# Performance work log

Hardware: AMD Instinct MI355X
Metric: run time of the kernel (lower is better)

The kernel has to match this reference:

```python
import jax, jax.numpy as jnp
import numpy as np

N, C, HEADS = 32768, 512, 8
CK = CV = C // 2   # key/value channels (= hidden//2 per AE.block1)
F2 = C // 2        # CAM in_features
BN_EPS = 1e-5


def _bn(x, p):
    # eval-mode BatchNorm2d on [n, c, w] (h=1 squeezed); p = [gamma, beta, mean, var] each [c]
    g, b, m, v = p
    inv = g / jnp.sqrt(v + BN_EPS)
    return (x - m[None, :, None]) * inv[None, :, None] + b[None, :, None]


def _conv(x, w):
    # 1x1 Conv2d (no bias) on [n, c, w]; w: [out_c, in_c]
    return jnp.einsum('ncw,oc->now', x, w)


def _block(x, y, ea_wk, ea_bk, ea_wq, ea_bq, ea_wv, ea_bv, ea_wr, ea_br,
           pool_w1, pool_bn1, pool_w2, pool_bn2,
           adapt_w1, adapt_bn1, adapt_w2, adapt_bn2,
           delta_w1, delta_bn1, delta_w2):
    # torch: input_ = stack([x, y]).permute([0,2,1]).unsqueeze(2) -> [2, C, 1, N]; we drop h=1 -> [2, C, N]
    inp = jnp.stack([x, y]).transpose(0, 2, 1)  # [2, C, N]

    # ---------------- EfficientAttention ----------------
    keys = _conv(inp, ea_wk) + ea_bk[None, :, None]      # [2, CK, N]
    queries = _conv(inp, ea_wq) + ea_bq[None, :, None]   # [2, CK, N]
    values = _conv(inp, ea_wv) + ea_bv[None, :, None]    # [2, CV, N]
    hk, hv = CK // HEADS, CV // HEADS
    K = jax.nn.softmax(keys.reshape(2, HEADS, hk, N), axis=-1)     # softmax over positions
    Q = jax.nn.softmax(queries.reshape(2, HEADS, hk, N), axis=2)   # softmax over head channels
    V = values.reshape(2, HEADS, hv, N)
    ctx = jnp.einsum('nhkw,nhvw->nhkv', K, V)                      # [2, H, hk, hv]
    att = jnp.einsum('nhkv,nhkw->nhvw', ctx, Q).reshape(2, CV, N)  # [2, CV, N]
    ea_full = _conv(att, ea_wr) + ea_br[None, :, None] + inp       # reprojection + residual
    ea_out = ((ea_full[0] + ea_full[1]) * 0.5).T                   # [N, C]

    # ---------------- CAM ----------------
    high = inp.mean(axis=2, keepdims=True)                 # AdaptiveAvgPool2d(1) -> [2, C, 1]
    high = _bn(_conv(high, pool_w1), pool_bn1)
    high = _bn(_conv(high, pool_w2), pool_bn2)             # [2, F2, 1]
    low = _bn(_conv(inp, adapt_w1), adapt_bn1)
    low = _bn(_conv(low, adapt_w2), adapt_bn2)             # [2, F2, N]
    # bilinear upsample of a 1x1 map == broadcast
    high_up = jnp.broadcast_to(high, (2, F2, N))
    concat = jnp.concatenate([low, high_up], axis=1)       # [2, 2*F2, N]
    d = _bn(_conv(concat, delta_w1), delta_bn1)
    delta = _conv(d, delta_w2)                             # [2, 2, N]: (dx, dy)
    # grid_sample of 1x1 `high`, zeros padding, align_corners=False; norm = [w/s, h/s] = [1, 1]
    gx = jnp.linspace(-1.0, 1.0, N)[None, :] + delta[:, 0]  # h_list + delta_x, [2, N]
    gy = -1.0 + delta[:, 1]                                 # linspace(-1,1,1) = -1
    ix, iy = gx * 0.5, gy * 0.5                             # unnormalized coords for W=H=1
    wgt = jnp.clip(1.0 - jnp.abs(ix), 0.0, 1.0) * jnp.clip(1.0 - jnp.abs(iy), 0.0, 1.0)  # [2, N]
    sampled = high * wgt[:, None, :]                        # [2, F2, N]
    cam_full = jnp.concatenate([sampled, low], axis=1)      # [2, 2*F2, N] == [2, C, N]
    cam_out = ((cam_full[0] + cam_full[1]) * 0.5).T         # [N, C]

    return (ea_out + cam_out) * 0.5                         # [N, C]


def setup_inputs() -> dict:
    key = jax.random.key(0)
    ks = iter(jax.random.split(key, 40))
    def rn(shape, s=0.05):
        return jax.random.normal(next(ks), shape, jnp.float32) * s
    def bn(c):
        p = jax.random.normal(next(ks), (4, c), jnp.float32) * 0.05
        p = p.at[0].add(1.0)                 # gamma ~ 1
        p = p.at[3].set(jnp.abs(p[3]) + 1.0)  # var > 0
        return p
    return {
        'x': jax.random.normal(next(ks), (N, C), jnp.float32),
        'y': jax.random.normal(next(ks), (N, C), jnp.float32),
        'ea_wk': rn((CK, C)), 'ea_bk': rn((CK,)),
        'ea_wq': rn((CK, C)), 'ea_bq': rn((CK,)),
        'ea_wv': rn((CV, C)), 'ea_bv': rn((CV,)),
        'ea_wr': rn((C, CV)), 'ea_br': rn((C,)),
        'pool_w1': rn((C, C)), 'pool_bn1': bn(C),
        'pool_w2': rn((F2, C)), 'pool_bn2': bn(F2),
        'adapt_w1': rn((C, C)), 'adapt_bn1': bn(C),
        'adapt_w2': rn((F2, C)), 'adapt_bn2': bn(F2),
        'delta_w1': rn((F2, 2 * F2)), 'delta_bn1': bn(F2),
        'delta_w2': rn((2, F2)),
    }


def reference(x, y, ea_wk, ea_bk, ea_wq, ea_bq, ea_wv, ea_bv, ea_wr, ea_br,
              pool_w1, pool_bn1, pool_w2, pool_bn2,
              adapt_w1, adapt_bn1, adapt_w2, adapt_bn2,
              delta_w1, delta_bn1, delta_w2):
    return _block(x, y, ea_wk, ea_bk, ea_wq, ea_bq, ea_wv, ea_bv, ea_wr, ea_br,
                  pool_w1, pool_bn1, pool_w2, pool_bn2,
                  adapt_w1, adapt_bn1, adapt_w2, adapt_bn2,
                  delta_w1, delta_bn1, delta_w2)
```

## Files before the change

### kernel.cpp

```cpp
#include <hip/hip_runtime.h>
#include <math.h>

#define B_CTXC   0
#define B_ZP     524288
#define B_COLS   526336
#define B_HIGH2  530432
#define B_CONSTD 532480
#define B_BIASO  532544
#define B_CPP    534592
#define B_CTXT   535616
#define B_WDD    568384
#define B_WDX    570432
#define B_WL     574528
#define B_WBIG   1098816
#define B_WKV    1639488
#define B_WR     2163776
#define B_PW1T   2425920
#define B_PW2T   3474496
#define B_D1BT   3998784

typedef __attribute__((ext_vector_type(8))) short bf16x8;
typedef __attribute__((ext_vector_type(4))) float f32x4;

#define MFMA(a, b, c) __builtin_amdgcn_mfma_f32_16x16x32_bf16(a, b, c, 0, 0, 0)
#define EVSWZ(row) ((((row) >> 1) & 3) << 4)

__device__ inline unsigned f2bfu(float f) {
  unsigned u = __float_as_uint(f);
  return (u + 0x7FFFu + ((u >> 16) & 1u)) >> 16;
}
__device__ inline unsigned pack2(float a, float b) { return f2bfu(a) | (f2bfu(b) << 16); }

__device__ inline void softmax_pack(f32x4 a0, f32x4 a1, const float* __restrict__ bq,
                                    int hh, int g, unsigned o[4]) {
  float q[8], e[8];
  float mx = -1e30f;
#pragma unroll
  for (int r = 0; r < 4; ++r) {
    q[r] = a0[r] + bq[hh * 32 + g * 4 + r];
    q[4 + r] = a1[r] + bq[hh * 32 + 16 + g * 4 + r];
    mx = fmaxf(mx, fmaxf(q[r], q[4 + r]));
  }
  mx = fmaxf(mx, __shfl_xor(mx, 16, 64));
  mx = fmaxf(mx, __shfl_xor(mx, 32, 64));
  float sm = 0.f;
#pragma unroll
  for (int r = 0; r < 8; ++r) { e[r] = __expf(q[r] - mx); sm += e[r]; }
  sm += __shfl_xor(sm, 16, 64);
  sm += __shfl_xor(sm, 32, 64);
  float inv = 1.f / sm;
  o[0] = pack2(e[0] * inv, e[1] * inv); o[1] = pack2(e[2] * inv, e[3] * inv);
  o[2] = pack2(e[4] * inv, e[5] * inv); o[3] = pack2(e[6] * inv, e[7] * inv);
}

__global__ __launch_bounds__(512) void kW1(
    const float* __restrict__ a1, const float* __restrict__ abn1,
    const float* __restrict__ a2, const float* __restrict__ abn2,
    char* __restrict__ wsb) {
  __shared__ float S1[512], F1[512], redu[512];
  const int t = threadIdx.x, o = blockIdx.x;
  float* wsf = (float*)wsb;
  {
    float gg = abn1[t], be = abn1[512 + t], mn = abn1[1024 + t], va = abn1[1536 + t];
    float s = gg * rsqrtf(va + 1e-5f);
    S1[t] = s; F1[t] = be - mn * s;
  }
  float g2 = abn2[o], be2 = abn2[256 + o], mn2 = abn2[512 + o], va2 = abn2[768 + o];
  float s2 = g2 * rsqrtf(va2 + 1e-5f);
  float f2v = be2 - mn2 * s2;
  __syncthreads();
  float acc = 0.f;
  const float* a2r = a2 + o * 512;
  for (int m = 0; m < 512; ++m) acc = fmaf(a2r[m] * S1[m], a1[m * 512 + t], acc);
  wsf[(B_WL / 4) + o * 512 + t] = s2 * acc;
  redu[t] = a2r[t] * F1[t];
  __syncthreads();
  for (int sft = 256; sft >= 1; sft >>= 1) {
    if (t < sft) redu[t] += redu[t + sft];
    __syncthreads();
  }
  if (t == 0) wsf[(B_CPP / 4) + o] = s2 * redu[0] + f2v;
}

__global__ __launch_bounds__(512) void kW2(
    const float* __restrict__ d1, const float* __restrict__ dbn1,
    const float* __restrict__ d2, char* __restrict__ wsb) {
  __shared__ float SD[256], WDDl[512];
  const int t = threadIdx.x;
  float* wsf = (float*)wsb;
  if (t < 256) {
    float gg = dbn1[t], va = dbn1[768 + t];
    SD[t] = gg * rsqrtf(va + 1e-5f);
  }
  __syncthreads();
  {
    int j = t >> 8, v = t & 255;
    float acc = 0.f;
    for (int o = 0; o < 256; ++o) acc = fmaf(d2[j * 256 + o] * SD[o], d1[o * 512 + v], acc);
    WDDl[t] = acc;
    wsf[(B_WDD / 4) + t] = acc;
  }
  __syncthreads();
  {
    int c = t;
    float acc0 = 0.f, acc1 = 0.f;
    for (int v = 0; v < 256; ++v) {
      float wl = wsf[(B_WL / 4) + v * 512 + c];
      acc0 = fmaf(WDDl[v], wl, acc0);
      acc1 = fmaf(WDDl[256 + v], wl, acc1);
    }
    wsf[(B_WDX / 4) + c] = acc0;
    wsf[(B_WDX / 4) + 512 + c] = acc1;
  }
}

__global__ __launch_bounds__(256) void kPack(
    const float* __restrict__ wq, const float* __restrict__ wk, const float* __restrict__ wv,
    const float* __restrict__ wr, const float* __restrict__ pw1, const float* __restrict__ pw2,
    const float* __restrict__ d1, char* __restrict__ wsb) {
  int i = blockIdx.x * 256 + threadIdx.x;
  float* wsf = (float*)wsb;
  unsigned short* u16 = (unsigned short*)wsb;
  if (i < 270336) {
    int T = i >> 13, r = i & 8191;
    int ks = r >> 9, l = (r >> 3) & 63, j = r & 7;
    int row = T * 16 + (l & 15);
    int col = ks * 32 + (l >> 4) * 8 + j;
    float v;
    if (row < 256) v = wq[row * 512 + col];
    else if (row < 512) v = wsf[(B_WL / 4) + (row - 256) * 512 + col];
    else if (row < 514) v = wsf[(B_WDX / 4) + (row - 512) * 512 + col];
    else v = 0.f;
    u16[(B_WBIG / 2) + i] = (unsigned short)f2bfu(v);
    return;
  }
  i -= 270336;
  if (i < 262144) {
    int T = i >> 13, r = i & 8191;
    int ks = r >> 9, l = (r >> 3) & 63, j = r & 7;
    int row = T * 16 + (l & 15);
    int col = ks * 32 + (l >> 4) * 8 + j;
    float v = row < 256 ? wk[row * 512 + col] : wv[(row - 256) * 512 + col];
    u16[(B_WKV / 2) + i] = (unsigned short)f2bfu(v);
    return;
  }
  i -= 262144;
  if (i < 131072) {
    int T = i >> 12, r = i & 4095;
    int ks = r >> 9, l = (r >> 3) & 63, j = r & 7;
    int row = T * 16 + (l & 15);
    int col = ks * 32 + (l >> 4) * 8 + j;
    u16[(B_WR / 2) + i] = (unsigned short)f2bfu(wr[row * 256 + col]);
    return;
  }
  i -= 131072;
  if (i < 262144) { int o = i >> 9, c = i & 511; wsf[(B_PW1T / 4) + c * 512 + o] = pw1[i]; return; }
  i -= 262144;
  if (i < 131072) { int o = i >> 9, c = i & 511; wsf[(B_PW2T / 4) + c * 256 + o] = pw2[i]; return; }
  i -= 131072;
  if (i < 65536) { int o = i >> 8, v = i & 255; wsf[(B_D1BT / 4) + v * 256 + o] = d1[o * 512 + 256 + v]; }
}

__global__ __launch_bounds__(1024, 1) void k1_reduce(
    const float* __restrict__ x, const float* __restrict__ y,
    const float* __restrict__ bk, const float* __restrict__ bv,
    const char* __restrict__ wsb, float* __restrict__ outp) {
  __shared__ __align__(16) unsigned char Xl[32768];
  __shared__ __align__(16) unsigned char Yl[32768];
  __shared__ __align__(16) unsigned char EVl[65536];
  __shared__ float Red[1536];
  unsigned char* elx = EVl;
  unsigned char* ely = EVl + 16384;
  unsigned char* vlx = EVl + 32768;
  unsigned char* vly = EVl + 49152;
  float* PSf = (float*)EVl;
  const int t = threadIdx.x;
  const int tw = t >> 6, lo16 = t & 15, g = (t >> 4) & 3, l = t & 63;
  const char* Wkv = wsb + B_WKV;

  if (t < 512) Red[t] = 0.f;
  float csum[2][8];
#pragma unroll
  for (int b2 = 0; b2 < 2; ++b2)
#pragma unroll
    for (int i = 0; i < 8; ++i) csum[b2][i] = 0.f;
  const int n0 = blockIdx.x * 32;
  const int bbase0 = lo16 * 1024 + g * 16;
  const int bbase1 = bbase0 + 16384;
  const int bswz = (lo16 & 7) << 4;
  const int pp0 = lo16, pp1 = 16 + lo16;

#pragma unroll
  for (int r = 0; r < 2; ++r) {
    int chunk = r * 1024 + t;
    int prow = chunk >> 6, j = chunk & 63;
    const float* gx = x + (size_t)(n0 + prow) * 512 + j * 8;
    const float* gy = y + (size_t)(n0 + prow) * 512 + j * 8;
    float4 x0 = *(const float4*)gx, x1 = *(const float4*)(gx + 4);
    float4 y0 = *(const float4*)gy, y1 = *(const float4*)(gy + 4);
    csum[0][0] += x0.x; csum[0][1] += x0.y; csum[0][2] += x0.z; csum[0][3] += x0.w;
    csum[0][4] += x1.x; csum[0][5] += x1.y; csum[0][6] += x1.z; csum[0][7] += x1.w;
    csum[1][0] += y0.x; csum[1][1] += y0.y; csum[1][2] += y0.z; csum[1][3] += y0.w;
    csum[1][4] += y1.x; csum[1][5] += y1.y; csum[1][6] += y1.z; csum[1][7] += y1.w;
    int byte = (prow * 1024 + j * 16) ^ ((prow & 7) << 4);
    uint4 pk;
    pk.x = pack2(x0.x, x0.y); pk.y = pack2(x0.z, x0.w);
    pk.z = pack2(x1.x, x1.y); pk.w = pack2(x1.z, x1.w);
    *(uint4*)(Xl + byte) = pk;
    pk.x = pack2(y0.x, y0.y); pk.y = pack2(y0.z, y0.w);
    pk.z = pack2(y1.x, y1.y); pk.w = pack2(y1.z, y1.w);
    *(uint4*)(Yl + byte) = pk;
  }
#pragma unroll
  for (int b = 0; b < 2; ++b)
#pragma unroll
    for (int i = 0; i < 8; ++i) PSf[t * 16 + b * 8 + i] = csum[b][i];
  __syncthreads();
  {
    int s = t, b = s >> 9, ch = s & 511, tlow = ch >> 3, ii = ch & 7;
    float sum = 0.f;
#pragma unroll
    for (int w2 = 0; w2 < 16; ++w2) sum += PSf[(w2 * 64 + tlow) * 16 + b * 8 + ii];
    Red[512 + s] = sum;
  }
  __syncthreads();

  f32x4 ax0p0 = {0,0,0,0}, ax0p1 = {0,0,0,0}, ay0p0 = {0,0,0,0}, ay0p1 = {0,0,0,0};
  f32x4 ax1p0 = {0,0,0,0}, ax1p1 = {0,0,0,0}, ay1p0 = {0,0,0,0}, ay1p1 = {0,0,0,0};
  {
    int t0 = tw * 2;
    const char* ap = Wkv + t0 * 16384 + l * 16;
#pragma unroll
    for (int ks = 0; ks < 16; ++ks) {
      bf16x8 bx0 = *(const bf16x8*)(Xl + ((bbase0 + ks * 64) ^ bswz));
      bf16x8 bx1 = *(const bf16x8*)(Xl + ((bbase1 + ks * 64) ^ bswz));
      bf16x8 by0 = *(const bf16x8*)(Yl + ((bbase0 + ks * 64) ^ bswz));
      bf16x8 by1 = *(const bf16x8*)(Yl + ((bbase1 + ks * 64) ^ bswz));
      bf16x8 af0 = *(const bf16x8*)(ap + ks * 1024);
      bf16x8 af1 = *(const bf16x8*)(ap + 16384 + ks * 1024);
      ax0p0 = MFMA(af0, bx0, ax0p0); ax0p1 = MFMA(af0, bx1, ax0p1);
      ay0p0 = MFMA(af0, by0, ay0p0); ay0p1 = MFMA(af0, by1, ay0p1);
      ax1p0 = MFMA(af1, bx0, ax1p0); ax1p1 = MFMA(af1, bx1, ax1p1);
      ay1p0 = MFMA(af1, by0, ay1p0); ay1p1 = MFMA(af1, by1, ay1p1);
    }
  }
  if (tw < 8) {
    int t0 = tw * 2, t1 = t0 + 1;
#pragma unroll
    for (int pt2 = 0; pt2 < 2; ++pt2) {
      f32x4 Ax0 = pt2 ? ax0p1 : ax0p0, Ax1 = pt2 ? ax1p1 : ax1p0;
      f32x4 Ay0 = pt2 ? ay0p1 : ay0p0, Ay1 = pt2 ? ay1p1 : ay1p0;
      int pp = pt2 ? pp1 : pp0;
      float ex0[4], ex1[4], ey0[4], ey1[4];
#pragma unroll
      for (int r = 0; r < 4; ++r) {
        float bk0 = bk[t0 * 16 + g * 4 + r], bk1 = bk[t1 * 16 + g * 4 + r];
        ex0[r] = __expf(Ax0[r] + bk0); ey0[r] = __expf(Ay0[r] + bk0);
        ex1[r] = __expf(Ax1[r] + bk1); ey1[r] = __expf(Ay1[r] + bk1);
      }
#pragma unroll
      for (int r = 0; r < 4; ++r) {
        float v0 = ex0[r], v1 = ex1[r], v2 = ey0[r], v3 = ey1[r];
        for (int m = 8; m >= 1; m >>= 1) {
          v0 += __shfl_xor(v0, m, 16); v1 += __shfl_xor(v1, m, 16);
          v2 += __shfl_xor(v2, m, 16); v3 += __shfl_xor(v3, m, 16);
        }
        if (lo16 == 0) {
          atomicAdd(&Red[t0 * 16 + g * 4 + r], v0);
          atomicAdd(&Red[t1 * 16 + g * 4 + r], v1);
          atomicAdd(&Red[256 + t0 * 16 + g * 4 + r], v2);
          atomicAdd(&Red[256 + t1 * 16 + g * 4 + r], v3);
        }
      }
#pragma unroll
      for (int r = 0; r < 4; ++r) {
        int row0 = t0 * 16 + g * 4 + r;
        int row1 = t1 * 16 + g * 4 + r;
        int a0 = (row0 * 64 + pp * 2) ^ EVSWZ(row0);
        int a1 = (row1 * 64 + pp * 2) ^ EVSWZ(row1);
        *(unsigned short*)(elx + a0) = (unsigned short)f2bfu(ex0[r]);
        *(unsigned short*)(elx + a1) = (unsigned short)f2bfu(ex1[r]);
        *(unsigned short*)(ely + a0) = (unsigned short)f2bfu(ey0[r]);
        *(unsigned short*)(ely + a1) = (unsigned short)f2bfu(ey1[r]);
      }
    }
  } else {
    int t0 = tw * 2, t1 = t0 + 1;
#pragma unroll
    for (int pt2 = 0; pt2 < 2; ++pt2) {
      f32x4 Ax0 = pt2 ? ax0p1 : ax0p0, Ax1 = pt2 ? ax1p1 : ax1p0;
      f32x4 Ay0 = pt2 ? ay0p1 : ay0p0, Ay1 = pt2 ? ay1p1 : ay1p0;
      int pp = pt2 ? pp1 : pp0;
#pragma unroll
      for (int r = 0; r < 4; ++r) {
        int row0 = (t0 - 16) * 16 + g * 4 + r;
        int row1 = (t1 - 16) * 16 + g * 4 + r;
        float bv0 = bv[row0], bv1 = bv[row1];
        int a0 = (row0 * 64 + pp * 2) ^ EVSWZ(row0);
        int a1 = (row1 * 64 + pp * 2) ^ EVSWZ(row1);
        *(unsigned short*)(vlx + a0) = (unsigned short)f2bfu(Ax0[r] + bv0);
        *(unsigned short*)(vlx + a1) = (unsigned short)f2bfu(Ax1[r] + bv1);
        *(unsigned short*)(vly + a0) = (unsigned short)f2bfu(Ay0[r] + bv0);
        *(unsigned short*)(vly + a1) = (unsigned short)f2bfu(Ay1[r] + bv1);
      }
    }
  }
  __syncthreads();

  {
    const int h2 = tw & 7, bsel = tw >> 3;
    const unsigned char* el = bsel ? ely : elx;
    const unsigned char* vl = bsel ? vly : vlx;
    unsigned* ctxp = (unsigned*)outp + (size_t)blockIdx.x * 8192;
#pragma unroll
    for (int m = 0; m < 2; ++m) {
      int rowe = h2 * 32 + m * 16 + lo16;
      bf16x8 ea = *(const bf16x8*)(el + ((rowe * 64 + g * 16) ^ EVSWZ(rowe)));
      f32x4 c0 = {0.f, 0.f, 0.f, 0.f}, c1 = {0.f, 0.f, 0.f, 0.f};
      {
        int rowv = h2 * 32 + lo16;
        bf16x8 vb = *(const bf16x8*)(vl + ((rowv * 64 + g * 16) ^ EVSWZ(rowv)));
        c0 = MFMA(ea, vb, c0);
      }
      {
        int rowv = h2 * 32 + 16 + lo16;
        bf16x8 vb = *(const bf16x8*)(vl + ((rowv * 64 + g * 16) ^ EVSWZ(rowv)));
        c1 = MFMA(ea, vb, c1);
      }
#pragma unroll
      for (int r = 0; r < 4; ++r)
        ctxp[((bsel * 2 + m) * 4 + r) * 512 + h2 * 64 + l] = pack2(c0[r], c1[r]);
    }
    float* redp = outp + 8388608 + blockIdx.x * 1536;
    for (int i = t; i < 1536; i += 1024) redp[i] = Red[i];
  }
}

__global__ __launch_bounds__(512) void k1b(const float* __restrict__ outp, char* __restrict__ wsb) {
  __shared__ float R[512];
  const int t = threadIdx.x, blk = blockIdx.x;
  float* wsf = (float*)wsb;
  if (blk < 64) {
    int sl = t & 127, part = t >> 7;
    int slot = blk * 128 + sl;
    const unsigned* p = (const unsigned*)outp;
    float s0 = 0.f, s1 = 0.f;
    for (int c = part * 256; c < part * 256 + 256; ++c) {
      unsigned wv = p[(size_t)c * 8192 + slot];
      s0 += __uint_as_float(wv << 16);
      s1 += __uint_as_float(wv & 0xffff0000u);
    }
    R[sl * 4 + part] = s0;
    __syncthreads();
    float sum0 = R[sl * 4] + R[sl * 4 + 1] + R[sl * 4 + 2] + R[sl * 4 + 3];
    __syncthreads();
    R[sl * 4 + part] = s1;
    __syncthreads();
    float sum1 = R[sl * 4] + R[sl * 4 + 1] + R[sl * 4 + 2] + R[sl * 4 + 3];
    if (part == 0) {
      int t_ = slot & 511, bmr = slot >> 9;
      int r = bmr & 3, m = (bmr >> 2) & 1, b = bmr >> 3;
      int h = t_ >> 6, g = (t_ >> 4) & 3, lo16 = t_ & 15;
      int klocal = m * 16 + g * 4 + r;
      int base = ((b * 8 + h) * 32 + klocal) * 32;
      wsf[(B_CTXC / 4) + base + lo16] = sum0;
      wsf[(B_CTXC / 4) + base + 16 + lo16] = sum1;
    }
  } else {
    int j = (blk - 64) * 512 + t;
    const float* rp = outp + 8388608;
    float s = 0.f;
    for (int c = 0; c < 1024; ++c) s += rp[(size_t)c * 1536 + j];
    if (j < 512) wsf[(B_ZP / 4) + j] = s;
    else wsf[(B_COLS / 4) + (j - 512)] = s;
  }
}

__global__ __launch_bounds__(512) void k2_finalize(
    const float* __restrict__ pbn1, const float* __restrict__ pbn2,
    const float* __restrict__ dbn1, const float* __restrict__ d2,
    const float* __restrict__ ea_br, char* __restrict__ wsb) {
  __shared__ float HI[1024], H1[1024], H2l[512], VB[512], slot[4];
  const int t = threadIdx.x;
  float* wsf = (float*)wsb;
  unsigned short* u16 = (unsigned short*)wsb;
  for (int idx = t; idx < 16384; idx += 512) {
    float s = wsf[(B_CTXC / 4) + idx];
    int v = idx & 31, row = idx >> 5;
    int b = row >> 8, kr = row & 255;
    int hh = kr >> 5, kh = kr & 31;
    float val = s / wsf[(B_ZP / 4) + b * 256 + kr];
    int m = v >> 4;
    int lane = (v & 15) + ((kh >> 3) << 4);
    int j = kh & 7;
    u16[(B_CTXT / 2) + (((b * 8 + hh) * 2 + m) << 9) + lane * 8 + j] = (unsigned short)f2bfu(val);
  }
  if (t < 4) slot[t] = 0.f;
  for (int idx = t; idx < 1024; idx += 512) HI[idx] = wsf[(B_COLS / 4) + idx] * (1.f / 32768.f);
  __syncthreads();
  {
    int o = t;
    float gg = pbn1[o], be = pbn1[512 + o], mn = pbn1[1024 + o], va = pbn1[1536 + o];
    float sc = gg * rsqrtf(va + 1e-5f), sh = be - mn * sc;
    for (int b = 0; b < 2; ++b) {
      float acc = 0.f;
      for (int c = 0; c < 512; ++c) acc = fmaf(wsf[(B_PW1T / 4) + c * 512 + o], HI[b * 512 + c], acc);
      H1[b * 512 + o] = acc * sc + sh;
    }
  }
  __syncthreads();
  if (t < 256) {
    int o = t;
    float gg = pbn2[o], be = pbn2[256 + o], mn = pbn2[512 + o], va = pbn2[768 + o];
    float sc = gg * rsqrtf(va + 1e-5f), sh = be - mn * sc;
    for (int b = 0; b < 2; ++b) {
      float acc = 0.f;
      for (int c = 0; c < 512; ++c) acc = fmaf(wsf[(B_PW2T / 4) + c * 256 + o], H1[b * 512 + c], acc);
      float vv = acc * sc + sh;
      H2l[b * 256 + o] = vv;
      wsf[(B_HIGH2 / 4) + b * 256 + o] = vv;
    }
  }
  __syncthreads();
  if (t < 256) {
    int o = t;
    float gg = dbn1[o], be = dbn1[256 + o], mn = dbn1[512 + o], va = dbn1[768 + o];
    float sd = gg * rsqrtf(va + 1e-5f), fd = be - mn * sd;
    for (int b = 0; b < 2; ++b) {
      float acc = 0.f;
      for (int v = 0; v < 256; ++v) acc = fmaf(wsf[(B_D1BT / 4) + v * 256 + o], H2l[b * 256 + v], acc);
      VB[b * 256 + o] = sd * acc + fd;
    }
  }
  __syncthreads();
  if (t < 256) {
    int o = t;
    for (int b = 0; b < 2; ++b)
      for (int j = 0; j < 2; ++j) atomicAdd(&slot[b * 2 + j], d2[j * 256 + o] * VB[b * 256 + o]);
    float cp = wsf[(B_CPP / 4) + o];
    for (int j = 0; j < 2; ++j) {
      float w = wsf[(B_WDD / 4) + j * 256 + o] * cp;
      atomicAdd(&slot[0 + j], w);
      atomicAdd(&slot[2 + j], w);
    }
  }
  __syncthreads();
  if (t < 4) wsf[(B_CONSTD / 4) + t] = slot[t];
  {
    int o = t;
    float bb = 0.5f * ea_br[o];
    if (o >= 256) bb += 0.5f * wsf[(B_CPP / 4) + o - 256];
    wsf[(B_BIASO / 4) + o] = bb;
  }
}

__global__ __launch_bounds__(1024, 1) void k3_main(
    const float* __restrict__ x, const float* __restrict__ y,
    const float* __restrict__ bq, const char* __restrict__ wsb,
    float* __restrict__ out) {
  __shared__ __align__(16) unsigned char Xl[32768];
  __shared__ __align__(16) unsigned char Yl[32768];
  __shared__ __align__(16) unsigned char ACCb[65536];
  __shared__ __align__(16) unsigned char Ql[16384];
  __shared__ float wgtl[64];
  const int t = threadIdx.x;
  const int tw = t >> 6, lo16 = t & 15, g = (t >> 4) & 3, l = t & 63;
  const int n0 = blockIdx.x * 32;
  const char* Wbig = wsb + B_WBIG;
  const char* WRp = wsb + B_WR;
  const char* CTXT = wsb + B_CTXT;
  const float* wsf = (const float*)wsb;
  const int bbase0 = lo16 * 1024 + g * 16;
  const int bbase1 = bbase0 + 16384;
  const int bswz = (lo16 & 7) << 4;
  const int swzq = (lo16 & 7) << 4;

#pragma unroll
  for (int r = 0; r < 2; ++r) {
    int chunk = r * 1024 + t;
    int prow = chunk >> 6, j = chunk & 63;
    const float* gx = x + (size_t)(n0 + prow) * 512 + j * 8;
    const float* gy = y + (size_t)(n0 + prow) * 512 + j * 8;
    float4 x0 = *(const float4*)gx, x1 = *(const float4*)(gx + 4);
    float4 y0 = *(const float4*)gy, y1 = *(const float4*)(gy + 4);
    int byte = (prow * 1024 + j * 16) ^ ((prow & 7) << 4);
    uint4 pk;
    pk.x = pack2(x0.x, x0.y); pk.y = pack2(x0.z, x0.w);
    pk.z = pack2(x1.x, x1.y); pk.w = pack2(x1.z, x1.w);
    *(uint4*)(Xl + byte) = pk;
    pk.x = pack2(y0.x, y0.y); pk.y = pack2(y0.z, y0.w);
    pk.z = pack2(y1.x, y1.y); pk.w = pack2(y1.z, y1.w);
    *(uint4*)(Yl + byte) = pk;
    int abase = prow * 2048 + j * 32;
    int aswz = (prow & 7) << 4;
    f32x4 a0 = {0.25f * (x0.x + y0.x), 0.25f * (x0.y + y0.y), 0.25f * (x0.z + y0.z), 0.25f * (x0.w + y0.w)};
    f32x4 a1 = {0.25f * (x1.x + y1.x), 0.25f * (x1.y + y1.y), 0.25f * (x1.z + y1.z), 0.25f * (x1.w + y1.w)};
    *(f32x4*)(ACCb + (abase ^ aswz)) = a0;
    *(f32x4*)(ACCb + ((abase + 16) ^ aswz)) = a1;
  }
  __syncthreads();

  f32x4 ax0p0 = {0,0,0,0}, ax0p1 = {0,0,0,0}, ay0p0 = {0,0,0,0}, ay0p1 = {0,0,0,0};
  f32x4 ax1p0 = {0,0,0,0}, ax1p1 = {0,0,0,0}, ay1p0 = {0,0,0,0}, ay1p1 = {0,0,0,0};
  {
    int t0 = tw * 2;
    const char* ap = Wbig + t0 * 16384 + l * 16;
#pragma unroll
    for (int ks = 0; ks < 16; ++ks) {
      bf16x8 bx0 = *(const bf16x8*)(Xl + ((bbase0 + ks * 64) ^ bswz));
      bf16x8 bx1 = *(const bf16x8*)(Xl + ((bbase1 + ks * 64) ^ bswz));
      bf16x8 by0 = *(const bf16x8*)(Yl + ((bbase0 + ks * 64) ^ bswz));
      bf16x8 by1 = *(const bf16x8*)(Yl + ((bbase1 + ks * 64) ^ bswz));
      bf16x8 af0 = *(const bf16x8*)(ap + ks * 1024);
      bf16x8 af1 = *(const bf16x8*)(ap + 16384 + ks * 1024);
      ax0p0 = MFMA(af0, bx0, ax0p0); ax0p1 = MFMA(af0, bx1, ax0p1);
      ay0p0 = MFMA(af0, by0, ay0p0); ay0p1 = MFMA(af0, by1, ay0p1);
      ax1p0 = MFMA(af1, bx0, ax1p0); ax1p1 = MFMA(af1, bx1, ax1p1);
      ay1p0 = MFMA(af1, by0, ay1p0); ay1p1 = MFMA(af1, by1, ay1p1);
    }
  }

  unsigned Qy0[4], Qy1[4];

  if (tw < 8) {
    int hh = tw;
    unsigned o[4];
    softmax_pack(ax0p0, ax1p0, bq, hh, g, o);
    {
      int base_q = lo16 * 512 + hh * 64 + g * 8;
      uint2 w0; w0.x = o[0]; w0.y = o[1];
      uint2 w1; w1.x = o[2]; w1.y = o[3];
      *(uint2*)(Ql + (base_q ^ swzq)) = w0;
      *(uint2*)(Ql + ((base_q + 32) ^ swzq)) = w1;
    }
    softmax_pack(ay0p0, ay1p0, bq, hh, g, Qy0);
    softmax_pack(ax0p1, ax1p1, bq, hh, g, o);
    {
      int base_q = lo16 * 512 + hh * 64 + g * 8;
      uint2 w0; w0.x = o[0]; w0.y = o[1];
      uint2 w1; w1.x = o[2]; w1.y = o[3];
      *(uint2*)(Ql + 8192 + (base_q ^ swzq)) = w0;
      *(uint2*)(Ql + 8192 + ((base_q + 32) ^ swzq)) = w1;
    }
    softmax_pack(ay0p1, ay1p1, bq, hh, g, Qy1);
  } else {
    int tile0 = tw * 2 - 16;
#pragma unroll
    for (int pt2 = 0; pt2 < 2; ++pt2) {
      int row = pt2 * 16 + lo16;
      int rsw = (row & 7) << 4;
#pragma unroll
      for (int half = 0; half < 2; ++half) {
        f32x4 axs = half ? (pt2 ? ax1p1 : ax1p0) : (pt2 ? ax0p1 : ax0p0);
        f32x4 ays = half ? (pt2 ? ay1p1 : ay1p0) : (pt2 ? ay0p1 : ay0p0);
        int ch4 = 64 + (tile0 + half) * 4 + g;
        int ab = (row * 2048 + ch4 * 16) ^ rsw;
        f32x4 cur = *(const f32x4*)(ACCb + ab);
        cur += 0.25f * (axs + ays);
        *(f32x4*)(ACCb + ab) = cur;
      }
    }
  }

  if (tw == 15) {
    f32x4 adxp0 = {0,0,0,0}, adxp1 = {0,0,0,0}, adyp0 = {0,0,0,0}, adyp1 = {0,0,0,0};
    const char* ap = Wbig + 32 * 16384 + l * 16;
#pragma unroll
    for (int ks = 0; ks < 16; ++ks) {
      bf16x8 bx0 = *(const bf16x8*)(Xl + ((bbase0 + ks * 64) ^ bswz));
      bf16x8 bx1 = *(const bf16x8*)(Xl + ((bbase1 + ks * 64) ^ bswz));
      bf16x8 by0 = *(const bf16x8*)(Yl + ((bbase0 + ks * 64) ^ bswz));
      bf16x8 by1 = *(const bf16x8*)(Yl + ((bbase1 + ks * 64) ^ bswz));
      bf16x8 af = *(const bf16x8*)(ap + ks * 1024);
      adxp0 = MFMA(af, bx0, adxp0); adxp1 = MFMA(af, bx1, adxp1);
      adyp0 = MFMA(af, by0, adyp0); adyp1 = MFMA(af, by1, adyp1);
    }
    if (g == 0) {
#pragma unroll
      for (int pt2 = 0; pt2 < 2; ++pt2) {
        int pos = n0 + pt2 * 16 + lo16;
        float base_gx = -1.f + 2.f * (float)pos / 32767.f;
#pragma unroll
        for (int b = 0; b < 2; ++b) {
          f32x4 ad = b ? (pt2 ? adyp1 : adyp0) : (pt2 ? adxp1 : adxp0);
          float d0 = ad[0] + wsf[(B_CONSTD / 4) + b * 2 + 0];
          float d1 = ad[1] + wsf[(B_CONSTD / 4) + b * 2 + 1];
          float gxv = base_gx + d0;
          float gyv = -1.f + d1;
          float ix = gxv * 0.5f, iy = gyv * 0.5f;
          float wx = fminf(fmaxf(1.f - fabsf(ix), 0.f), 1.f);
          float wy = fminf(fmaxf(1.f - fabsf(iy), 0.f), 1.f);
          wgtl[b * 32 + pt2 * 16 + lo16] = wx * wy;
        }
      }
    }
  }

  if (tw < 8) {
    int hh = tw;
#pragma unroll
    for (int pt2 = 0; pt2 < 2; ++pt2) {
      unsigned char* Qs = Ql + pt2 * 8192;
      const unsigned* Qy = pt2 ? Qy1 : Qy0;
      f32x4 at0 = {0,0,0,0}, at1 = {0,0,0,0};
      {
        bf16x8 qf = *(const bf16x8*)(Qs + ((lo16 * 512 + hh * 64 + g * 16) ^ swzq));
        const char* cp = CTXT + (0 * 8 + hh) * 2048 + l * 16;
        bf16x8 c0 = *(const bf16x8*)(cp);
        bf16x8 c1 = *(const bf16x8*)(cp + 1024);
        at0 = MFMA(c0, qf, at0);
        at1 = MFMA(c1, qf, at1);
      }
      {
        int base_q = lo16 * 512 + hh * 64 + g * 8;
        uint2 w0; w0.x = Qy[0]; w0.y = Qy[1];
        uint2 w1; w1.x = Qy[2]; w1.y = Qy[3];
        *(uint2*)(Qs + (base_q ^ swzq)) = w0;
        *(uint2*)(Qs + ((base_q + 32) ^ swzq)) = w1;
      }
      {
        bf16x8 qf = *(const bf16x8*)(Qs + ((lo16 * 512 + hh * 64 + g * 16) ^ swzq));
        const char* cp = CTXT + (1 * 8 + hh) * 2048 + l * 16;
        bf16x8 c0 = *(const bf16x8*)(cp);
        bf16x8 c1 = *(const bf16x8*)(cp + 1024);
        at0 = MFMA(c0, qf, at0);
        at1 = MFMA(c1, qf, at1);
      }
#pragma unroll
      for (int m = 0; m < 2; ++m) {
        f32x4 v = m ? at1 : at0;
        uint2 wv;
        wv.x = pack2(v[0], v[1]); wv.y = pack2(v[2], v[3]);
        int byte = (lo16 * 512 + hh * 64 + m * 32 + g * 8) ^ swzq;
        *(uint2*)(Qs + byte) = wv;
      }
    }
  }
  __syncthreads();

  {
    int T0 = tw * 2;
    f32x4 r0p0 = {0,0,0,0}, r0p1 = {0,0,0,0}, r1p0 = {0,0,0,0}, r1p1 = {0,0,0,0};
    const char* ap = WRp + T0 * 8192 + l * 16;
#pragma unroll
    for (int ks = 0; ks < 8; ++ks) {
      bf16x8 br0 = *(const bf16x8*)(Ql + ((lo16 * 512 + g * 16 + ks * 64) ^ swzq));
      bf16x8 br1 = *(const bf16x8*)(Ql + 8192 + ((lo16 * 512 + g * 16 + ks * 64) ^ swzq));
      bf16x8 a0 = *(const bf16x8*)(ap + ks * 1024);
      bf16x8 a1 = *(const bf16x8*)(ap + 8192 + ks * 1024);
      r0p0 = MFMA(a0, br0, r0p0); r0p1 = MFMA(a0, br1, r0p1);
      r1p0 = MFMA(a1, br0, r1p0); r1p1 = MFMA(a1, br1, r1p1);
    }
#pragma unroll
    for (int pt2 = 0; pt2 < 2; ++pt2) {
      int row = pt2 * 16 + lo16;
      int rsw = (row & 7) << 4;
#pragma unroll
      for (int half = 0; half < 2; ++half) {
        f32x4 rr = half ? (pt2 ? r1p1 : r1p0) : (pt2 ? r0p1 : r0p0);
        int ch4 = (T0 + half) * 4 + g;
        int ab = (row * 2048 + ch4 * 16) ^ rsw;
        f32x4 cur = *(const f32x4*)(ACCb + ab);
        cur += 0.25f * rr;
        *(f32x4*)(ACCb + ab) = cur;
      }
    }
  }
  __syncthreads();

  const float* bo = wsf + (B_BIASO / 4);
#pragma unroll
  for (int i = 0; i < 4; ++i) {
    int idx = i * 1024 + t;
    int pos = idx >> 7, c4 = idx & 127;
    int ab = (pos * 2048 + c4 * 16) ^ ((pos & 7) << 4);
    f32x4 acc = *(const f32x4*)(ACCb + ab);
    f32x4 bb = *(const f32x4*)(bo + c4 * 4);
    if (c4 < 64) {
      f32x4 h20 = *(const f32x4*)(wsf + (B_HIGH2 / 4) + c4 * 4);
      f32x4 h21 = *(const f32x4*)(wsf + (B_HIGH2 / 4) + 256 + c4 * 4);
      float wg0 = wgtl[pos], wg1 = wgtl[32 + pos];
      acc += (0.25f * wg0) * h20 + (0.25f * wg1) * h21;
    }
    acc += bb;
    *(f32x4*)(out + (size_t)(n0 + pos) * 512 + c4 * 4) = acc;
  }
}

extern "C" void kernel_launch(void* const* d_in, const int* in_sizes, int n_in,
                              void* d_out, int out_size, void* d_ws, size_t ws_size,
                              hipStream_t stream) {
  const float* x = (const float*)d_in[0];
  const float* y = (const float*)d_in[1];
  const float* ea_wk = (const float*)d_in[2];
  const float* ea_bk = (const float*)d_in[3];
  const float* ea_wq = (const float*)d_in[4];
  const float* ea_bq = (const float*)d_in[5];
  const float* ea_wv = (const float*)d_in[6];
  const float* ea_bv = (const float*)d_in[7];
  const float* ea_wr = (const float*)d_in[8];
  const float* ea_br = (const float*)d_in[9];
  const float* pool_w1 = (const float*)d_in[10];
  const float* pool_bn1 = (const float*)d_in[11];
  const float* pool_w2 = (const float*)d_in[12];
  const float* pool_bn2 = (const float*)d_in[13];
  const float* adapt_w1 = (const float*)d_in[14];
  const float* adapt_bn1 = (const float*)d_in[15];
  const float* adapt_w2 = (const float*)d_in[16];
  const float* adapt_bn2 = (const float*)d_in[17];
  const float* delta_w1 = (const float*)d_in[18];
  const float* delta_bn1 = (const float*)d_in[19];
  const float* delta_w2 = (const float*)d_in[20];
  char* ws = (char*)d_ws;
  float* out = (float*)d_out;

  kW1<<<256, 512, 0, stream>>>(adapt_w1, adapt_bn1, adapt_w2, adapt_bn2, ws);
  kW2<<<1, 512, 0, stream>>>(delta_w1, delta_bn1, delta_w2, ws);
  kPack<<<4384, 256, 0, stream>>>(ea_wq, ea_wk, ea_wv, ea_wr, pool_w1, pool_w2, delta_w1, ws);
  k1_reduce<<<1024, 1024, 0, stream>>>(x, y, ea_bk, ea_bv, ws, out);
  k1b<<<67, 512, 0, stream>>>(out, ws);
  k2_finalize<<<1, 512, 0, stream>>>(pool_bn1, pool_bn2, delta_bn1, delta_w2, ea_br, ws);
  k3_main<<<1024, 1024, 0, stream>>>(x, y, ea_bq, ws, out);
}
```

Before: 359.7 us.

## Alias LDS buffers in k1_reduce to allow two resident blocks per CU

Merges the X/Y staging buffers and the exp/value/partial-sum buffers into one 64KB shared region and raises launch_bounds to two blocks per CU. To make the aliasing safe, the column-sum partial reduction and the bf16 stores of the exp values are moved after the MFMA phase behind extra barriers, with the exp values kept in registers in between. The aim is to roughly halve LDS use per block so more blocks can be resident and hide load latency. The costs are additional __syncthreads, more live registers, and possible spills under the tighter register cap that the second block per CU imposes.

```diff
diff --git a/kernel.cpp b/kernel.cpp
--- a/kernel.cpp
+++ b/kernel.cpp
@@ -161,19 +161,19 @@
   if (i < 65536) { int o = i >> 8, v = i & 255; wsf[(B_D1BT / 4) + v * 256 + o] = d1[o * 512 + 256 + v]; }
 }
 
-__global__ __launch_bounds__(1024, 1) void k1_reduce(
+__global__ __launch_bounds__(1024, 2) void k1_reduce(
     const float* __restrict__ x, const float* __restrict__ y,
     const float* __restrict__ bk, const float* __restrict__ bv,
     const char* __restrict__ wsb, float* __restrict__ outp) {
-  __shared__ __align__(16) unsigned char Xl[32768];
-  __shared__ __align__(16) unsigned char Yl[32768];
-  __shared__ __align__(16) unsigned char EVl[65536];
+  __shared__ __align__(16) unsigned char XYl[65536];
   __shared__ float Red[1536];
-  unsigned char* elx = EVl;
-  unsigned char* ely = EVl + 16384;
-  unsigned char* vlx = EVl + 32768;
-  unsigned char* vly = EVl + 49152;
-  float* PSf = (float*)EVl;
+  unsigned char* Xl = XYl;
+  unsigned char* Yl = XYl + 32768;
+  float* PSf = (float*)XYl;
+  unsigned char* elx = XYl;
+  unsigned char* ely = XYl + 16384;
+  unsigned char* vlx = XYl + 32768;
+  unsigned char* vly = XYl + 49152;
   const int t = threadIdx.x;
   const int tw = t >> 6, lo16 = t & 15, g = (t >> 4) & 3, l = t & 63;
   const char* Wkv = wsb + B_WKV;
@@ -211,18 +211,6 @@
     pk.z = pack2(y1.x, y1.y); pk.w = pack2(y1.z, y1.w);
     *(uint4*)(Yl + byte) = pk;
   }
-#pragma unroll
-  for (int b = 0; b < 2; ++b)
-#pragma unroll
-    for (int i = 0; i < 8; ++i) PSf[t * 16 + b * 8 + i] = csum[b][i];
-  __syncthreads();
-  {
-    int s = t, b = s >> 9, ch = s & 511, tlow = ch >> 3, ii = ch & 7;
-    float sum = 0.f;
-#pragma unroll
-    for (int w2 = 0; w2 < 16; ++w2) sum += PSf[(w2 * 64 + tlow) * 16 + b * 8 + ii];
-    Red[512 + s] = sum;
-  }
   __syncthreads();
 
   f32x4 ax0p0 = {0,0,0,0}, ax0p1 = {0,0,0,0}, ay0p0 = {0,0,0,0}, ay0p1 = {0,0,0,0};
@@ -244,23 +232,22 @@
       ay1p0 = MFMA(af1, by0, ay1p0); ay1p1 = MFMA(af1, by1, ay1p1);
     }
   }
+  float ex0[2][4], ex1[2][4], ey0[2][4], ey1[2][4];
   if (tw < 8) {
     int t0 = tw * 2, t1 = t0 + 1;
 #pragma unroll
     for (int pt2 = 0; pt2 < 2; ++pt2) {
       f32x4 Ax0 = pt2 ? ax0p1 : ax0p0, Ax1 = pt2 ? ax1p1 : ax1p0;
       f32x4 Ay0 = pt2 ? ay0p1 : ay0p0, Ay1 = pt2 ? ay1p1 : ay1p0;
-      int pp = pt2 ? pp1 : pp0;
-      float ex0[4], ex1[4], ey0[4], ey1[4];
 #pragma unroll
       for (int r = 0; r < 4; ++r) {
         float bk0 = bk[t0 * 16 + g * 4 + r], bk1 = bk[t1 * 16 + g * 4 + r];
-        ex0[r] = __expf(Ax0[r] + bk0); ey0[r] = __expf(Ay0[r] + bk0);
-        ex1[r] = __expf(Ax1[r] + bk1); ey1[r] = __expf(Ay1[r] + bk1);
+        ex0[pt2][r] = __expf(Ax0[r] + bk0); ey0[pt2][r] = __expf(Ay0[r] + bk0);
+        ex1[pt2][r] = __expf(Ax1[r] + bk1); ey1[pt2][r] = __expf(Ay1[r] + bk1);
       }
 #pragma unroll
       for (int r = 0; r < 4; ++r) {
-        float v0 = ex0[r], v1 = ex1[r], v2 = ey0[r], v3 = ey1[r];
+        float v0 = ex0[pt2][r], v1 = ex1[pt2][r], v2 = ey0[pt2][r], v3 = ey1[pt2][r];
         for (int m = 8; m >= 1; m >>= 1) {
           v0 += __shfl_xor(v0, m, 16); v1 += __shfl_xor(v1, m, 16);
           v2 += __shfl_xor(v2, m, 16); v3 += __shfl_xor(v3, m, 16);
@@ -272,16 +259,39 @@
           atomicAdd(&Red[256 + t1 * 16 + g * 4 + r], v3);
         }
       }
+    }
+  }
+  __syncthreads();
+
+#pragma unroll
+  for (int b = 0; b < 2; ++b)
+#pragma unroll
+    for (int i = 0; i < 8; ++i) PSf[t * 16 + b * 8 + i] = csum[b][i];
+  __syncthreads();
+  {
+    int s = t, b = s >> 9, ch = s & 511, tlow = ch >> 3, ii = ch & 7;
+    float sum = 0.f;
+#pragma unroll
+    for (int w2 = 0; w2 < 16; ++w2) sum += PSf[(w2 * 64 + tlow) * 16 + b * 8 + ii];
+    Red[512 + s] = sum;
+  }
+  __syncthreads();
+
+  if (tw < 8) {
+    int t0 = tw * 2, t1 = t0 + 1;
+#pragma unroll
+    for (int pt2 = 0; pt2 < 2; ++pt2) {
+      int pp = pt2 ? pp1 : pp0;
 #pragma unroll
       for (int r = 0; r < 4; ++r) {
         int row0 = t0 * 16 + g * 4 + r;
         int row1 = t1 * 16 + g * 4 + r;
         int a0 = (row0 * 64 + pp * 2) ^ EVSWZ(row0);
         int a1 = (row1 * 64 + pp * 2) ^ EVSWZ(row1);
-        *(unsigned short*)(elx + a0) = (unsigned short)f2bfu(ex0[r]);
-        *(unsigned short*)(elx + a1) = (unsigned short)f2bfu(ex1[r]);
-        *(unsigned short*)(ely + a0) = (unsigned short)f2bfu(ey0[r]);
-        *(unsigned short*)(ely + a1) = (unsigned short)f2bfu(ey1[r]);
+        *(unsigned short*)(elx + a0) = (unsigned short)f2bfu(ex0[pt2][r]);
+        *(unsigned short*)(elx + a1) = (unsigned short)f2bfu(ex1[pt2][r]);
+        *(unsigned short*)(ely + a0) = (unsigned short)f2bfu(ey0[pt2][r]);
+        *(unsigned short*)(ely + a1) = (unsigned short)f2bfu(ey1[pt2][r]);
       }
     }
   } else {
```

After: 368.2 us. 1.02x slower.
